# Kernel optimization log

Hardware: AMD Instinct MI355X
Metric: run time of the kernel (lower is better)

The kernel has to match this reference:

```python
import jax, jax.numpy as jnp
import numpy as np

MODEL_DIM = 1024
NUM_HEADS = 16
HEAD_DIM = MODEL_DIM // NUM_HEADS
B, L = 2, 2048


def setup_inputs() -> dict:
    key = jax.random.key(0)
    ks = jax.random.split(key, 11)
    s = 1.0 / np.sqrt(MODEL_DIM)
    inp = {
        "q": jax.random.normal(ks[0], (B, L, MODEL_DIM), jnp.float32),
        "k": jax.random.normal(ks[1], (B, L, MODEL_DIM), jnp.float32),
        "v": jax.random.normal(ks[2], (B, L, MODEL_DIM), jnp.float32),
        "Wq": jax.random.uniform(ks[3], (MODEL_DIM, MODEL_DIM), jnp.float32, -s, s),
        "bq": jax.random.uniform(ks[4], (MODEL_DIM,), jnp.float32, -s, s),
        "Wk": jax.random.uniform(ks[5], (MODEL_DIM, MODEL_DIM), jnp.float32, -s, s),
        "bk": jax.random.uniform(ks[6], (MODEL_DIM,), jnp.float32, -s, s),
        "Wv": jax.random.uniform(ks[7], (MODEL_DIM, MODEL_DIM), jnp.float32, -s, s),
        "bv": jax.random.uniform(ks[8], (MODEL_DIM,), jnp.float32, -s, s),
        "Wo": jax.random.uniform(ks[9], (MODEL_DIM, MODEL_DIM), jnp.float32, -s, s),
        "bo": jax.random.uniform(ks[10], (MODEL_DIM,), jnp.float32, -s, s),
    }
    return inp


def reference(q, k, v, Wq, bq, Wk, bk, Wv, bv, Wo, bo):
    Bq, Lq, D = q.shape
    H, Hd = NUM_HEADS, HEAD_DIM
    # Linear projections (torch Linear: x @ W.T + b)
    Q = q @ Wq.T + bq
    K = k @ Wk.T + bk
    V = v @ Wv.T + bv
    # split heads -> [B, H, L, Hd]
    def split(x):
        return x.reshape(Bq, Lq, H, Hd).transpose(0, 2, 1, 3)
    Qh, Kh, Vh = split(Q), split(K), split(V)
    scale = 1.0 / jnp.sqrt(jnp.asarray(Hd, Q.dtype))
    scores = jnp.einsum("bhqd,bhkd->bhqk", Qh, Kh) * scale
    attn = jax.nn.softmax(scores, axis=-1)  # dropout = identity in eval
    ctx = jnp.einsum("bhqk,bhkd->bhqd", attn, Vh)
    ctx = ctx.transpose(0, 2, 1, 3).reshape(Bq, Lq, D)
    return ctx @ Wo.T + bo
```

## Files before the change

kernel.cpp:

```cpp
#include <hip/hip_runtime.h>


typedef __attribute__((ext_vector_type(4))) float f32x4;
typedef __attribute__((ext_vector_type(16))) float f32x16;
typedef __attribute__((ext_vector_type(4))) unsigned int u32x4;
typedef __attribute__((ext_vector_type(2))) unsigned int u32x2;
typedef __attribute__((ext_vector_type(8))) short bf16x8;

#define DEVI static __device__ __forceinline__

DEVI unsigned short f2bf(float x) {
  union { float f; unsigned u; } v; v.f = x;
  unsigned r = v.u + 0x7fffu + ((v.u >> 16) & 1u);
  return (unsigned short)(r >> 16);
}

DEVI unsigned cvtpk(float lo, float hi) {
  unsigned r;
  asm("v_cvt_pk_bf16_f32 %0, %1, %2" : "=v"(r) : "v"(lo), "v"(hi));
  return r;
}

DEVI float exp2v(float x) {
  float y;
  asm("v_exp_f32 %0, %1" : "=v"(y) : "v"(x));
  return y;
}

DEVI void gload_lds16(const void* g, void* l) {
  __builtin_amdgcn_global_load_lds((__attribute__((address_space(1))) void*)g,
                                   (__attribute__((address_space(3))) void*)l, 16, 0, 0);
}

#define WAIT_VM(N) asm volatile("s_waitcnt vmcnt(" #N ")" ::: "memory")
#define WAIT_LGKM0 asm volatile("s_waitcnt lgkmcnt(0)" ::: "memory")
#define BARRIER __builtin_amdgcn_s_barrier()

constexpr int MD = 1024;
constexpr int NH = 16;
constexpr int HD = 64;
constexpr int LL = 2048;
constexpr float CQ = 0.18033688011112042f;
constexpr float CREF = 8.0f;

struct CvtArgs { const float* src[4]; unsigned short* dst[4]; };

__global__ void cvt_kernel(CvtArgs a) {
  const int which = blockIdx.x >> 9;
  const int i = ((blockIdx.x & 511) * 256 + threadIdx.x) * 8;
  const float* w = a.src[which];
  unsigned short* o = a.dst[which];
  f32x4 x = *(const f32x4*)(w + i);
  f32x4 y = *(const f32x4*)(w + i + 4);
  union { unsigned u[4]; u32x4 q; } r;
  r.u[0] = cvtpk(x[0], x[1]); r.u[1] = cvtpk(x[2], x[3]);
  r.u[2] = cvtpk(y[0], y[1]); r.u[3] = cvtpk(y[2], y[3]);
  *(u32x4*)(o + i) = r.q;
}

struct QKVArgs {
  const float* A[3];
  const unsigned short* W[3];
  const float* bias[3];
  unsigned short* out[3];
};

__global__ __launch_bounds__(256, 3) void gemm_qkv(QKVArgs args) {
  __shared__ alignas(16) unsigned short SM[24576];
  unsigned short* const Ab_ = SM;
  unsigned short* const Bb_ = SM + 12288;

  const int tid = threadIdx.x;
  const int lane = tid & 63;
  const int wave = tid >> 6;
  const int wr = wave >> 1, wc = wave & 1;
  const int lr = lane & 15, lg = lane >> 4;

  const int logical = (int)(blockIdx.x & 7) * 96 + (int)(blockIdx.x >> 3);
  const int n0 = (logical & 7) * 128;
  const int y = logical >> 3;
  const int mode = y >> 5;
  const int m0 = (y & 31) * 128;

  const float* Af = args.A[mode];
  const unsigned short* Wb = args.W[mode];
  const float* bias = args.bias[mode];
  unsigned short* Out = args.out[mode];

  const int arow = tid >> 1;
  const int ahalf = tid & 1;
  const int rrow = lane >> 2, rslot = lane & 3;

  f32x4 acc[4][4] = {};
  f32x4 areg[4];

  auto loadA = [&](int kt) {
    const float* s = Af + (size_t)(m0 + arow) * 1024 + kt * 32 + ahalf * 16;
    areg[0] = *(const f32x4*)(s);
    areg[1] = *(const f32x4*)(s + 4);
    areg[2] = *(const f32x4*)(s + 8);
    areg[3] = *(const f32x4*)(s + 12);
  };

  auto stageW = [&](int slot, int kt) {
    const int k0 = kt * 32;
    #pragma unroll
    for (int sh = 0; sh < 2; ++sh) {
      const int row = sh * 64 + wave * 16 + rrow;
      const int ss = rslot ^ ((row >> 1) & 3);
      gload_lds16((const char*)(Wb + (size_t)(n0 + row) * 1024 + k0) + ss * 16,
                  (char*)(Bb_ + slot * 4096) + sh * 4096 + wave * 1024);
    }
  };

  auto writeA = [&](int slot) {
    const int x = (arow >> 1) & 3;
    union { unsigned u[4]; u32x4 q; } t0, t1;
    t0.u[0] = cvtpk(areg[0][0], areg[0][1]); t0.u[1] = cvtpk(areg[0][2], areg[0][3]);
    t0.u[2] = cvtpk(areg[1][0], areg[1][1]); t0.u[3] = cvtpk(areg[1][2], areg[1][3]);
    t1.u[0] = cvtpk(areg[2][0], areg[2][1]); t1.u[1] = cvtpk(areg[2][2], areg[2][3]);
    t1.u[2] = cvtpk(areg[3][0], areg[3][1]); t1.u[3] = cvtpk(areg[3][2], areg[3][3]);
    char* base = (char*)(Ab_ + slot * 4096) + arow * 64;
    *(u32x4*)(base + (((unsigned)(2 * ahalf)     ^ x) << 4)) = t0.q;
    *(u32x4*)(base + (((unsigned)(2 * ahalf + 1) ^ x) << 4)) = t1.q;
  };

  loadA(0); stageW(0, 0);
  writeA(0);
  loadA(1); stageW(1, 1);

  int slot = 0;
  for (int kt = 0; kt < 32; ++kt) {
    if (kt < 31) WAIT_VM(6);
    else         WAIT_VM(0);
    WAIT_LGKM0;
    BARRIER;

    const int slot1 = (slot + 1 >= 3) ? slot - 2 : slot + 1;
    const int slot2 = (slot + 2 >= 3) ? slot - 1 : slot + 2;
    if (kt < 31) writeA(slot1);
    if (kt < 30) { loadA(kt + 2); stageW(slot2, kt + 2); }

    bf16x8 af[4], bfr[4];
    #pragma unroll
    for (int mi = 0; mi < 4; ++mi) {
      const int row = wr * 64 + mi * 16 + lr;
      af[mi] = *(const bf16x8*)((const char*)(Ab_ + slot * 4096) + row * 64 +
                                (((unsigned)lg ^ ((row >> 1) & 3)) << 4));
    }
    #pragma unroll
    for (int ni = 0; ni < 4; ++ni) {
      const int row = wc * 64 + ni * 16 + lr;
      bfr[ni] = *(const bf16x8*)((const char*)(Bb_ + slot * 4096) + row * 64 +
                                 (((unsigned)lg ^ ((row >> 1) & 3)) << 4));
    }
    #pragma unroll
    for (int mi = 0; mi < 4; ++mi)
      #pragma unroll
      for (int ni = 0; ni < 4; ++ni)
        acc[mi][ni] = __builtin_amdgcn_mfma_f32_16x16x32_bf16(af[mi], bfr[ni], acc[mi][ni], 0, 0, 0);

    slot = slot1;
  }

  float bv[4];
  const int cn = n0 + wc * 64 + lr;
  #pragma unroll
  for (int ni = 0; ni < 4; ++ni) bv[ni] = bias[cn + ni * 16];

  if (mode == 2) {
    BARRIER;
    constexpr int TP = 136;
    #pragma unroll
    for (int mi = 0; mi < 4; ++mi) {
      #pragma unroll
      for (int ni = 0; ni < 4; ++ni) {
        const int nloc = wc * 64 + lr + ni * 16;
        const int mloc = wr * 64 + mi * 16 + lg * 4;
        union { unsigned short us[4]; u32x2 u; } p;
        #pragma unroll
        for (int j = 0; j < 4; ++j) p.us[j] = f2bf(acc[mi][ni][j] + bv[ni]);
        *(u32x2*)(SM + nloc * TP + mloc) = p.u;
      }
    }
    WAIT_LGKM0;
    BARRIER;
    const int nloc = tid >> 1;
    const int mh = (tid & 1) * 64;
    const int ng = n0 + nloc;
    const int h = ng >> 6, d = ng & 63;
    const int bidx = m0 >> 11;
    const int l0 = (m0 & 2047) + mh;
    unsigned short* op = Out + ((size_t)(bidx * NH + h) * HD + d) * LL + l0;
    const unsigned short* src = SM + nloc * TP + mh;
    #pragma unroll
    for (int e = 0; e < 8; ++e)
      *(u32x4*)(op + e * 8) = *(const u32x4*)(src + e * 8);
  } else {
    #pragma unroll
    for (int mi = 0; mi < 4; ++mi) {
      #pragma unroll
      for (int j = 0; j < 4; ++j) {
        const int m = m0 + wr * 64 + mi * 16 + lg * 4 + j;
        const int b = m >> 11, l = m & 2047;
        #pragma unroll
        for (int ni = 0; ni < 4; ++ni) {
          const int n = cn + ni * 16;
          const int h = n >> 6, d = n & 63;
          float val = acc[mi][ni][j] + bv[ni];
          if (mode == 0) val *= CQ;
          Out[((size_t)(b * NH + h) * LL + l) * HD + d] = f2bf(val);
        }
      }
    }
  }
}

__global__ __launch_bounds__(256, 4) void gemm_out(const unsigned short* __restrict__ Ab,
                                                   const unsigned short* __restrict__ Wb,
                                                   const float* __restrict__ bias,
                                                   float* __restrict__ Out) {
  __shared__ alignas(16) unsigned short Abuf[3][128 * 32];
  __shared__ alignas(16) unsigned short Bbuf[3][64 * 32];

  const int tid = threadIdx.x;
  const int lane = tid & 63;
  const int wave = tid >> 6;
  const int wr = wave >> 1, wc = wave & 1;
  const int lr = lane & 15, lg = lane >> 4;

  const int logical = (int)(blockIdx.x & 7) * 64 + (int)(blockIdx.x >> 3);
  const int n0 = (logical & 15) * 64;
  const int m0 = (logical >> 4) * 128;

  const int rrow = lane >> 2, rslot = lane & 3;

  f32x4 acc[4][2] = {};

  auto stage = [&](int slot, int kt) {
    const int k0 = kt * 32;
    #pragma unroll
    for (int sh = 0; sh < 2; ++sh) {
      const int row = sh * 64 + wave * 16 + rrow;
      const int ss = rslot ^ ((row >> 1) & 3);
      gload_lds16((const char*)(Ab + (size_t)(m0 + row) * 1024 + k0) + ss * 16,
                  (char*)&Abuf[slot][0] + sh * 4096 + wave * 1024);
    }
    {
      const int row = wave * 16 + rrow;
      const int ss = rslot ^ ((row >> 1) & 3);
      gload_lds16((const char*)(Wb + (size_t)(n0 + row) * 1024 + k0) + ss * 16,
                  (char*)&Bbuf[slot][0] + wave * 1024);
    }
  };

  stage(0, 0); stage(1, 1);

  int slot = 0;
  for (int kt = 0; kt < 32; ++kt) {
    if (kt < 31) WAIT_VM(3);
    else         WAIT_VM(0);
    BARRIER;
    if (kt < 30) stage((slot + 2 >= 3) ? slot - 1 : slot + 2, kt + 2);

    bf16x8 af[4], bfr[2];
    #pragma unroll
    for (int mi = 0; mi < 4; ++mi) {
      const int row = wr * 64 + mi * 16 + lr;
      af[mi] = *(const bf16x8*)((const char*)&Abuf[slot][0] + row * 64 +
                                (((unsigned)lg ^ ((row >> 1) & 3)) << 4));
    }
    #pragma unroll
    for (int ni = 0; ni < 2; ++ni) {
      const int row = wc * 32 + ni * 16 + lr;
      bfr[ni] = *(const bf16x8*)((const char*)&Bbuf[slot][0] + row * 64 +
                                 (((unsigned)lg ^ ((row >> 1) & 3)) << 4));
    }
    #pragma unroll
    for (int mi = 0; mi < 4; ++mi)
      #pragma unroll
      for (int ni = 0; ni < 2; ++ni)
        acc[mi][ni] = __builtin_amdgcn_mfma_f32_16x16x32_bf16(af[mi], bfr[ni], acc[mi][ni], 0, 0, 0);

    slot = (slot + 1 >= 3) ? 0 : slot + 1;
  }

  float bv[2];
  const int cn = n0 + wc * 32 + lr;
  #pragma unroll
  for (int ni = 0; ni < 2; ++ni) bv[ni] = bias[cn + ni * 16];

  #pragma unroll
  for (int mi = 0; mi < 4; ++mi)
    #pragma unroll
    for (int j = 0; j < 4; ++j) {
      const int m = m0 + wr * 64 + mi * 16 + lg * 4 + j;
      #pragma unroll
      for (int ni = 0; ni < 2; ++ni)
        Out[(size_t)m * 1024 + cn + ni * 16] = acc[mi][ni][j] + bv[ni];
    }
}

__global__ __launch_bounds__(256, 2) void attn_kernel(const unsigned short* __restrict__ Qh,
                                                      const unsigned short* __restrict__ Kh,
                                                      const unsigned short* __restrict__ Vt,
                                                      unsigned short* __restrict__ Ctx) {
  constexpr int KB = 64;
  constexpr int NT = LL / KB;
  __shared__ alignas(16) unsigned short Kl[3][KB * HD];
  __shared__ alignas(16) unsigned short Vl[3][HD * KB];

  const int tid = threadIdx.x;
  const int lane = tid & 63;
  const int wave = tid >> 6;
  const int lq = lane & 31;
  const int hi = lane >> 5;

  const int logical = (int)(blockIdx.x & 7) * 64 + (int)(blockIdx.x >> 3);
  const int bh = logical >> 4;
  const int q0 = (logical & 15) * 128 + wave * 32;

  const unsigned short* Kg = Kh + (size_t)bh * LL * HD;
  const unsigned short* Vg = Vt + (size_t)bh * HD * LL;

  bf16x8 qf[4];
  {
    const unsigned short* qp = Qh + (size_t)bh * LL * HD + (size_t)(q0 + lq) * HD + hi * 8;
    #pragma unroll
    for (int s = 0; s < 4; ++s) qf[s] = *(const bf16x8*)(qp + s * 16);
  }

  f32x16 oacc0 = {}, oacc1 = {};
  float s_ = 0.f;

  auto stage = [&](int slot, int t) {
    #pragma unroll
    for (int shot = 0; shot < 2; ++shot) {
      const int o = shot * 4096 + tid * 16;
      const int row = o >> 7, col = o & 127;
      const int sc = col ^ ((row & 7) << 4);
      gload_lds16((const char*)Kg + (size_t)(t * KB + row) * (HD * 2) + sc,
                  (char*)&Kl[slot][0] + shot * 4096 + wave * 1024);
    }
    #pragma unroll
    for (int shot = 0; shot < 2; ++shot) {
      const int o = shot * 4096 + tid * 16;
      const int row = o >> 7, col = o & 127;
      const int sc = col ^ ((row & 7) << 4);
      gload_lds16((const char*)Vg + (size_t)row * (LL * 2) + t * (KB * 2) + sc,
                  (char*)&Vl[slot][0] + shot * 4096 + wave * 1024);
    }
  };

  stage(0, 0); stage(1, 1);

  int slot = 0;
  for (int t = 0; t < NT; ++t) {
    if (t < NT - 1) WAIT_VM(4);
    else            WAIT_VM(0);
    BARRIER;
    if (t < NT - 2) stage((slot + 2 >= 3) ? slot - 1 : slot + 2, t + 2);

    const int swz = (lq & 7) << 4;

    bf16x8 kf0[4], kf1[4], vf0[4], vf1[4];
    #pragma unroll
    for (int s = 0; s < 4; ++s) {
      const int off = ((s * 32 + hi * 16) ^ swz);
      kf0[s] = *(const bf16x8*)((const char*)&Kl[slot][0] + lq * 128 + off);
      kf1[s] = *(const bf16x8*)((const char*)&Kl[slot][0] + (32 + lq) * 128 + off);
    }
    #pragma unroll
    for (int s = 0; s < 4; ++s) {
      const int off = ((s * 32 + hi * 16) ^ swz);
      vf0[s] = *(const bf16x8*)((const char*)&Vl[slot][0] + lq * 128 + off);
      vf1[s] = *(const bf16x8*)((const char*)&Vl[slot][0] + (32 + lq) * 128 + off);
    }

    f32x16 st0 = {}, st1 = {};
    __builtin_amdgcn_s_setprio(1);
    #pragma unroll
    for (int s = 0; s < 4; ++s) {
      st0 = __builtin_amdgcn_mfma_f32_32x32x16_bf16(kf0[s], qf[s], st0, 0, 0, 0);
      st1 = __builtin_amdgcn_mfma_f32_32x32x16_bf16(kf1[s], qf[s], st1, 0, 0, 0);
    }
    __builtin_amdgcn_s_setprio(0);

    float a4[4] = {0.f, 0.f, 0.f, 0.f};
    #pragma unroll
    for (int i = 0; i < 16; ++i) {
      float y0 = exp2v(st0[i] - CREF);
      float y1 = exp2v(st1[i] - CREF);
      st0[i] = y0; st1[i] = y1;
      a4[i & 3] += y0; a4[i & 3] += y1;
    }
    s_ += (a4[0] + a4[1]) + (a4[2] + a4[3]);

    bf16x8 pfr[4];
    #pragma unroll
    for (int s = 0; s < 4; ++s) {
      const int r = (s & 1) * 8;
      float p0, p1, p2, p3, p4, p5, p6, p7;
      if (s < 2) {
        p0 = st0[r+0]; p1 = st0[r+1]; p2 = st0[r+2]; p3 = st0[r+3];
        p4 = st0[r+4]; p5 = st0[r+5]; p6 = st0[r+6]; p7 = st0[r+7];
      } else {
        p0 = st1[r+0]; p1 = st1[r+1]; p2 = st1[r+2]; p3 = st1[r+3];
        p4 = st1[r+4]; p5 = st1[r+5]; p6 = st1[r+6]; p7 = st1[r+7];
      }
      unsigned a0 = cvtpk(p0, p1);
      unsigned a1 = cvtpk(p2, p3);
      unsigned a2 = cvtpk(p4, p5);
      unsigned a3 = cvtpk(p6, p7);
      asm volatile("v_permlane32_swap_b32 %0, %1" : "+v"(a0), "+v"(a2));
      asm volatile("v_permlane32_swap_b32 %0, %1" : "+v"(a1), "+v"(a3));
      union { unsigned u[4]; bf16x8 v; } pf;
      pf.u[0] = a0;
      pf.u[1] = a1;
      pf.u[2] = a2;
      pf.u[3] = a3;
      pfr[s] = pf.v;
    }

    __builtin_amdgcn_s_setprio(1);
    #pragma unroll
    for (int s = 0; s < 4; ++s) {
      oacc0 = __builtin_amdgcn_mfma_f32_32x32x16_bf16(vf0[s], pfr[s], oacc0, 0, 0, 0);
      oacc1 = __builtin_amdgcn_mfma_f32_32x32x16_bf16(vf1[s], pfr[s], oacc1, 0, 0, 0);
    }
    __builtin_amdgcn_s_setprio(0);

    slot = (slot + 1 >= 3) ? 0 : slot + 1;
  }

  s_ += __shfl_xor(s_, 32);
  const float inv = 1.0f / s_;
  const int b = bh >> 4, h = bh & 15;
  const int q = q0 + lq;
  unsigned short* op = Ctx + ((size_t)(b * LL + q)) * MD + h * HD;
  #pragma unroll
  for (int g = 0; g < 4; ++g) {
    {
      union { unsigned short us[4]; u32x2 u; } w;
      #pragma unroll
      for (int j = 0; j < 4; ++j) w.us[j] = f2bf(oacc0[g * 4 + j] * inv);
      *(u32x2*)(op + 8 * g + 4 * hi) = w.u;
    }
    {
      union { unsigned short us[4]; u32x2 u; } w;
      #pragma unroll
      for (int j = 0; j < 4; ++j) w.us[j] = f2bf(oacc1[g * 4 + j] * inv);
      *(u32x2*)(op + 32 + 8 * g + 4 * hi) = w.u;
    }
  }
}

extern "C" void kernel_launch(void* const* d_in, const int* in_sizes, int n_in,
                              void* d_out, int out_size, void* d_ws, size_t ws_size,
                              hipStream_t stream) {
  const float* q  = (const float*)d_in[0];
  const float* k  = (const float*)d_in[1];
  const float* v  = (const float*)d_in[2];
  const float* Wq = (const float*)d_in[3];
  const float* bq = (const float*)d_in[4];
  const float* Wk = (const float*)d_in[5];
  const float* bk = (const float*)d_in[6];
  const float* Wv = (const float*)d_in[7];
  const float* bv = (const float*)d_in[8];
  const float* Wo = (const float*)d_in[9];
  const float* bo = (const float*)d_in[10];

  char* ws = (char*)d_ws;
  const size_t MB = 1u << 20;
  unsigned short* Wqb = (unsigned short*)(ws + 0 * MB);
  unsigned short* Wkb = (unsigned short*)(ws + 2 * MB);
  unsigned short* Wvb = (unsigned short*)(ws + 4 * MB);
  unsigned short* Wob = (unsigned short*)(ws + 6 * MB);
  unsigned short* Qhb = (unsigned short*)(ws + 8 * MB);
  unsigned short* Khb = (unsigned short*)(ws + 16 * MB);
  unsigned short* Vtb = (unsigned short*)(ws + 24 * MB);
  unsigned short* ctx = (unsigned short*)(ws + 32 * MB);

  CvtArgs ca;
  ca.src[0] = Wq; ca.src[1] = Wk; ca.src[2] = Wv; ca.src[3] = Wo;
  ca.dst[0] = Wqb; ca.dst[1] = Wkb; ca.dst[2] = Wvb; ca.dst[3] = Wob;
  cvt_kernel<<<2048, 256, 0, stream>>>(ca);

  QKVArgs args;
  args.A[0] = q;  args.A[1] = k;  args.A[2] = v;
  args.W[0] = Wqb; args.W[1] = Wkb; args.W[2] = Wvb;
  args.bias[0] = bq; args.bias[1] = bk; args.bias[2] = bv;
  args.out[0] = Qhb; args.out[1] = Khb; args.out[2] = Vtb;
  gemm_qkv<<<768, 256, 0, stream>>>(args);

  attn_kernel<<<512, 256, 0, stream>>>(Qhb, Khb, Vtb, ctx);

  gemm_out<<<512, 256, 0, stream>>>(ctx, Wob, bo, (float*)d_out);
}
```

Baseline: 119.5 us.

## Software-pipeline QK^T of next tile with softmax and PV of current tile

Restructures the attention loop so the QK^T MFMAs for tile t+1 are issued before the exp/softmax and PV work of tile t, letting matrix and vector work interleave. This requires waiting for all outstanding loads (WAIT_VM(0)) each iteration instead of allowing one stage in flight. It also raises register pressure from carrying two score accumulators. The stricter wait may expose global-load latency that the triple buffering previously hid.

```diff
diff --git a/kernel.cpp b/kernel.cpp
--- a/kernel.cpp
+++ b/kernel.cpp
@@ -354,37 +354,61 @@
 
   stage(0, 0); stage(1, 1);
 
+  const int swz = (lq & 7) << 4;
+  f32x16 st0, st1;
   int slot = 0;
+
   for (int t = 0; t < NT; ++t) {
-    if (t < NT - 1) WAIT_VM(4);
-    else            WAIT_VM(0);
+    WAIT_VM(0);
     BARRIER;
-    if (t < NT - 2) stage((slot + 2 >= 3) ? slot - 1 : slot + 2, t + 2);
-
-    const int swz = (lq & 7) << 4;
-
-    bf16x8 kf0[4], kf1[4], vf0[4], vf1[4];
-    #pragma unroll
-    for (int s = 0; s < 4; ++s) {
-      const int off = ((s * 32 + hi * 16) ^ swz);
-      kf0[s] = *(const bf16x8*)((const char*)&Kl[slot][0] + lq * 128 + off);
-      kf1[s] = *(const bf16x8*)((const char*)&Kl[slot][0] + (32 + lq) * 128 + off);
-    }
+    const int slot1 = (slot + 1 >= 3) ? slot - 2 : slot + 1;
+    const int slot2 = (slot + 2 >= 3) ? slot - 1 : slot + 2;
+    if (t < NT - 2) stage(slot2, t + 2);
+
+    if (t == 0) {
+      bf16x8 k00[4], k01[4];
+      #pragma unroll
+      for (int s = 0; s < 4; ++s) {
+        const int off = ((s * 32 + hi * 16) ^ swz);
+        k00[s] = *(const bf16x8*)((const char*)&Kl[0][0] + lq * 128 + off);
+        k01[s] = *(const bf16x8*)((const char*)&Kl[0][0] + (32 + lq) * 128 + off);
+      }
+      f32x16 a = {}, b = {};
+      __builtin_amdgcn_s_setprio(1);
+      #pragma unroll
+      for (int s = 0; s < 4; ++s) {
+        a = __builtin_amdgcn_mfma_f32_32x32x16_bf16(k00[s], qf[s], a, 0, 0, 0);
+        b = __builtin_amdgcn_mfma_f32_32x32x16_bf16(k01[s], qf[s], b, 0, 0, 0);
+      }
+      __builtin_amdgcn_s_setprio(0);
+      st0 = a; st1 = b;
+    }
+
+    bf16x8 vf0[4], vf1[4];
     #pragma unroll
     for (int s = 0; s < 4; ++s) {
       const int off = ((s * 32 + hi * 16) ^ swz);
       vf0[s] = *(const bf16x8*)((const char*)&Vl[slot][0] + lq * 128 + off);
       vf1[s] = *(const bf16x8*)((const char*)&Vl[slot][0] + (32 + lq) * 128 + off);
     }
-
-    f32x16 st0 = {}, st1 = {};
-    __builtin_amdgcn_s_setprio(1);
-    #pragma unroll
-    for (int s = 0; s < 4; ++s) {
-      st0 = __builtin_amdgcn_mfma_f32_32x32x16_bf16(kf0[s], qf[s], st0, 0, 0, 0);
-      st1 = __builtin_amdgcn_mfma_f32_32x32x16_bf16(kf1[s], qf[s], st1, 0, 0, 0);
-    }
-    __builtin_amdgcn_s_setprio(0);
+    bf16x8 kf0[4], kf1[4];
+    if (t < NT - 1) {
+      #pragma unroll
+      for (int s = 0; s < 4; ++s) {
+        const int off = ((s * 32 + hi * 16) ^ swz);
+        kf0[s] = *(const bf16x8*)((const char*)&Kl[slot1][0] + lq * 128 + off);
+        kf1[s] = *(const bf16x8*)((const char*)&Kl[slot1][0] + (32 + lq) * 128 + off);
+      }
+    }
+
+    f32x16 nst0 = {}, nst1 = {};
+    if (t < NT - 1) {
+      #pragma unroll
+      for (int s = 0; s < 4; ++s) {
+        nst0 = __builtin_amdgcn_mfma_f32_32x32x16_bf16(kf0[s], qf[s], nst0, 0, 0, 0);
+        nst1 = __builtin_amdgcn_mfma_f32_32x32x16_bf16(kf1[s], qf[s], nst1, 0, 0, 0);
+      }
+    }
 
     float a4[4] = {0.f, 0.f, 0.f, 0.f};
     #pragma unroll
@@ -430,7 +454,8 @@
     }
     __builtin_amdgcn_s_setprio(0);
 
-    slot = (slot + 1 >= 3) ? 0 : slot + 1;
+    st0 = nst0; st1 = nst1;
+    slot = slot1;
   }
 
   s_ += __shfl_xor(s_, 32);
```

Result: no change. 121.9 us (+2.0%).

## Use 128-key tiles with double buffering and a new V swizzle in attention

Applied to the files above, without the earlier changes.

The attention kernel now processes 128 keys per iteration instead of 64, with two LDS buffers instead of a three-deep ring. It prefetches only one tile ahead and waits for all outstanding loads each iteration. The V tile row is now 256 bytes, so the V LDS swizzle is rewritten to XOR 16-byte slots with the low four bits of d. This halves the number of barriers and loop iterations, but it shortens the prefetch distance and keeps four score accumulators live, which raises register pressure.

```diff
diff --git a/kernel.cpp b/kernel.cpp
--- a/kernel.cpp
+++ b/kernel.cpp
@@ -305,10 +305,10 @@
                                                       const unsigned short* __restrict__ Kh,
                                                       const unsigned short* __restrict__ Vt,
                                                       unsigned short* __restrict__ Ctx) {
-  constexpr int KB = 64;
+  constexpr int KB = 128;
   constexpr int NT = LL / KB;
-  __shared__ alignas(16) unsigned short Kl[3][KB * HD];
-  __shared__ alignas(16) unsigned short Vl[3][HD * KB];
+  __shared__ alignas(16) unsigned short Kl[2][KB * HD];
+  __shared__ alignas(16) unsigned short Vl[2][HD * KB];
 
   const int tid = threadIdx.x;
   const int lane = tid & 63;
@@ -333,104 +333,111 @@
   f32x16 oacc0 = {}, oacc1 = {};
   float s_ = 0.f;
 
-  auto stage = [&](int slot, int t) {
-    #pragma unroll
-    for (int shot = 0; shot < 2; ++shot) {
+  auto stage = [&](int buf, int t) {
+    #pragma unroll
+    for (int shot = 0; shot < 4; ++shot) {
       const int o = shot * 4096 + tid * 16;
       const int row = o >> 7, col = o & 127;
       const int sc = col ^ ((row & 7) << 4);
       gload_lds16((const char*)Kg + (size_t)(t * KB + row) * (HD * 2) + sc,
-                  (char*)&Kl[slot][0] + shot * 4096 + wave * 1024);
-    }
-    #pragma unroll
-    for (int shot = 0; shot < 2; ++shot) {
+                  (char*)&Kl[buf][0] + shot * 4096 + wave * 1024);
+    }
+    #pragma unroll
+    for (int shot = 0; shot < 4; ++shot) {
       const int o = shot * 4096 + tid * 16;
-      const int row = o >> 7, col = o & 127;
-      const int sc = col ^ ((row & 7) << 4);
-      gload_lds16((const char*)Vg + (size_t)row * (LL * 2) + t * (KB * 2) + sc,
-                  (char*)&Vl[slot][0] + shot * 4096 + wave * 1024);
+      const int d = o >> 8;
+      const int slot16 = (o & 255) >> 4;
+      const int sc = ((slot16 ^ (d & 15)) << 4);
+      gload_lds16((const char*)Vg + (size_t)d * (LL * 2) + t * (KB * 2) + sc,
+                  (char*)&Vl[buf][0] + shot * 4096 + wave * 1024);
     }
   };
 
-  stage(0, 0); stage(1, 1);
-
-  int slot = 0;
+  stage(0, 0);
+
+  const int swz = (lq & 7) << 4;
   for (int t = 0; t < NT; ++t) {
-    if (t < NT - 1) WAIT_VM(4);
-    else            WAIT_VM(0);
+    const int buf = t & 1;
+    WAIT_VM(0);
     BARRIER;
-    if (t < NT - 2) stage((slot + 2 >= 3) ? slot - 1 : slot + 2, t + 2);
-
-    const int swz = (lq & 7) << 4;
-
-    bf16x8 kf0[4], kf1[4], vf0[4], vf1[4];
-    #pragma unroll
-    for (int s = 0; s < 4; ++s) {
-      const int off = ((s * 32 + hi * 16) ^ swz);
-      kf0[s] = *(const bf16x8*)((const char*)&Kl[slot][0] + lq * 128 + off);
-      kf1[s] = *(const bf16x8*)((const char*)&Kl[slot][0] + (32 + lq) * 128 + off);
-    }
-    #pragma unroll
-    for (int s = 0; s < 4; ++s) {
-      const int off = ((s * 32 + hi * 16) ^ swz);
-      vf0[s] = *(const bf16x8*)((const char*)&Vl[slot][0] + lq * 128 + off);
-      vf1[s] = *(const bf16x8*)((const char*)&Vl[slot][0] + (32 + lq) * 128 + off);
-    }
-
-    f32x16 st0 = {}, st1 = {};
-    __builtin_amdgcn_s_setprio(1);
-    #pragma unroll
-    for (int s = 0; s < 4; ++s) {
-      st0 = __builtin_amdgcn_mfma_f32_32x32x16_bf16(kf0[s], qf[s], st0, 0, 0, 0);
-      st1 = __builtin_amdgcn_mfma_f32_32x32x16_bf16(kf1[s], qf[s], st1, 0, 0, 0);
-    }
-    __builtin_amdgcn_s_setprio(0);
-
-    float a4[4] = {0.f, 0.f, 0.f, 0.f};
-    #pragma unroll
-    for (int i = 0; i < 16; ++i) {
-      float y0 = exp2v(st0[i] - CREF);
-      float y1 = exp2v(st1[i] - CREF);
-      st0[i] = y0; st1[i] = y1;
-      a4[i & 3] += y0; a4[i & 3] += y1;
-    }
-    s_ += (a4[0] + a4[1]) + (a4[2] + a4[3]);
-
-    bf16x8 pfr[4];
-    #pragma unroll
-    for (int s = 0; s < 4; ++s) {
-      const int r = (s & 1) * 8;
-      float p0, p1, p2, p3, p4, p5, p6, p7;
-      if (s < 2) {
-        p0 = st0[r+0]; p1 = st0[r+1]; p2 = st0[r+2]; p3 = st0[r+3];
-        p4 = st0[r+4]; p5 = st0[r+5]; p6 = st0[r+6]; p7 = st0[r+7];
-      } else {
-        p0 = st1[r+0]; p1 = st1[r+1]; p2 = st1[r+2]; p3 = st1[r+3];
-        p4 = st1[r+4]; p5 = st1[r+5]; p6 = st1[r+6]; p7 = st1[r+7];
-      }
-      unsigned a0 = cvtpk(p0, p1);
-      unsigned a1 = cvtpk(p2, p3);
-      unsigned a2 = cvtpk(p4, p5);
-      unsigned a3 = cvtpk(p6, p7);
-      asm volatile("v_permlane32_swap_b32 %0, %1" : "+v"(a0), "+v"(a2));
-      asm volatile("v_permlane32_swap_b32 %0, %1" : "+v"(a1), "+v"(a3));
-      union { unsigned u[4]; bf16x8 v; } pf;
-      pf.u[0] = a0;
-      pf.u[1] = a1;
-      pf.u[2] = a2;
-      pf.u[3] = a3;
-      pfr[s] = pf.v;
-    }
-
-    __builtin_amdgcn_s_setprio(1);
-    #pragma unroll
-    for (int s = 0; s < 4; ++s) {
-      oacc0 = __builtin_amdgcn_mfma_f32_32x32x16_bf16(vf0[s], pfr[s], oacc0, 0, 0, 0);
-      oacc1 = __builtin_amdgcn_mfma_f32_32x32x16_bf16(vf1[s], pfr[s], oacc1, 0, 0, 0);
-    }
-    __builtin_amdgcn_s_setprio(0);
-
-    slot = (slot + 1 >= 3) ? 0 : slot + 1;
+    if (t + 1 < NT) stage(buf ^ 1, t + 1);
+
+    f32x16 st[4];
+    #pragma unroll
+    for (int kb = 0; kb < 4; ++kb) {
+      bf16x8 kf[4];
+      #pragma unroll
+      for (int s = 0; s < 4; ++s) {
+        const int row = kb * 32 + lq;
+        kf[s] = *(const bf16x8*)((const char*)&Kl[buf][0] + row * 128 +
+                                 ((s * 32 + hi * 16) ^ swz));
+      }
+      f32x16 a = {};
+      __builtin_amdgcn_s_setprio(1);
+      #pragma unroll
+      for (int s = 0; s < 4; ++s)
+        a = __builtin_amdgcn_mfma_f32_32x32x16_bf16(kf[s], qf[s], a, 0, 0, 0);
+      __builtin_amdgcn_s_setprio(0);
+      st[kb] = a;
+    }
+
+    #pragma unroll
+    for (int hf = 0; hf < 2; ++hf) {
+      bf16x8 vf0[4], vf1[4];
+      #pragma unroll
+      for (int s = 0; s < 4; ++s) {
+        const int sl = (2 * (4 * hf + s) + hi);
+        const int d0 = lq, d1 = 32 + lq;
+        vf0[s] = *(const bf16x8*)((const char*)&Vl[buf][0] + d0 * 256 +
+                                  ((unsigned)(sl ^ (d0 & 15)) << 4));
+        vf1[s] = *(const bf16x8*)((const char*)&Vl[buf][0] + d1 * 256 +
+                                  ((unsigned)(sl ^ (d1 & 15)) << 4));
+      }
+
+      f32x16& st0 = st[2 * hf];
+      f32x16& st1 = st[2 * hf + 1];
+
+      float a4[4] = {0.f, 0.f, 0.f, 0.f};
+      #pragma unroll
+      for (int i = 0; i < 16; ++i) {
+        float y0 = exp2v(st0[i] - CREF);
+        float y1 = exp2v(st1[i] - CREF);
+        st0[i] = y0; st1[i] = y1;
+        a4[i & 3] += y0; a4[i & 3] += y1;
+      }
+      s_ += (a4[0] + a4[1]) + (a4[2] + a4[3]);
+
+      bf16x8 pfr[4];
+      #pragma unroll
+      for (int s = 0; s < 4; ++s) {
+        const int r = (s & 1) * 8;
+        float p0, p1, p2, p3, p4, p5, p6, p7;
+        if (s < 2) {
+          p0 = st0[r+0]; p1 = st0[r+1]; p2 = st0[r+2]; p3 = st0[r+3];
+          p4 = st0[r+4]; p5 = st0[r+5]; p6 = st0[r+6]; p7 = st0[r+7];
+        } else {
+          p0 = st1[r+0]; p1 = st1[r+1]; p2 = st1[r+2]; p3 = st1[r+3];
+          p4 = st1[r+4]; p5 = st1[r+5]; p6 = st1[r+6]; p7 = st1[r+7];
+        }
+        unsigned a0 = cvtpk(p0, p1);
+        unsigned a1 = cvtpk(p2, p3);
+        unsigned a2 = cvtpk(p4, p5);
+        unsigned a3 = cvtpk(p6, p7);
+        asm volatile("v_permlane32_swap_b32 %0, %1" : "+v"(a0), "+v"(a2));
+        asm volatile("v_permlane32_swap_b32 %0, %1" : "+v"(a1), "+v"(a3));
+        union { unsigned u[4]; bf16x8 v; } pf;
+        pf.u[0] = a0; pf.u[1] = a1; pf.u[2] = a2; pf.u[3] = a3;
+        pfr[s] = pf.v;
+      }
+
+      __builtin_amdgcn_s_setprio(1);
+      #pragma unroll
+      for (int s = 0; s < 4; ++s) {
+        oacc0 = __builtin_amdgcn_mfma_f32_32x32x16_bf16(vf0[s], pfr[s], oacc0, 0, 0, 0);
+        oacc1 = __builtin_amdgcn_mfma_f32_32x32x16_bf16(vf1[s], pfr[s], oacc1, 0, 0, 0);
+      }
+      __builtin_amdgcn_s_setprio(0);
+    }
   }
 
   s_ += __shfl_xor(s_, 32);
```

Result: no change. 120.7 us (+1.0%).
